# Optimization experiments

Hardware: AMD Instinct MI355X
Metric: run time of the kernel (lower is better)

## Reference

```python
import jax, jax.numpy as jnp
import numpy as np

N = 100000
E = 3200000
IN_DIM = 512
HID = 256
NUM_CLASSES = 16
P_DROP = 0.5
EPS_BN = 1e-5


def setup_inputs() -> dict:
    key = jax.random.key(0)
    ks = jax.random.split(key, 6)
    x = jax.random.normal(ks[0], (N, IN_DIM), jnp.float32)
    edge_src = jax.random.randint(ks[1], (E,), 0, N, dtype=jnp.int32)
    edge_dst = jax.random.randint(ks[2], (E,), 0, N, dtype=jnp.int32)
    # Glorot-ish init for GraphConv weights (bias=False in the module)
    W1 = jax.random.normal(ks[3], (IN_DIM, HID), jnp.float32) / np.sqrt(IN_DIM).astype(np.float32)
    W2 = jax.random.normal(ks[4], (HID, NUM_CLASSES), jnp.float32) / np.sqrt(HID).astype(np.float32)
    W3 = jax.random.normal(ks[5], (HID, NUM_CLASSES), jnp.float32) / np.sqrt(HID).astype(np.float32)
    return {"x": x, "W1": W1, "W2": W2, "W3": W3,
            "edge_src": edge_src, "edge_dst": edge_dst}


def _graph_conv(h, W, edge_src, edge_dst, out_inv_sqrt, in_inv_sqrt):
    # DGL GraphConv, norm='both', bias=False:
    #   rst = D_in^{-1/2} * A_agg( D_out^{-1/2} * h @ W )
    # Apply W before aggregation (out_dim <= in_dim here); same math as DGL.
    h = h * out_inv_sqrt[:, None]          # [N, d_in]
    h = h @ W                              # [N, d_out]
    agg = jax.ops.segment_sum(h[edge_src], edge_dst, num_segments=h.shape[0])
    return agg * in_inv_sqrt[:, None]


def _dropout(key, x, p=P_DROP):
    keep = jax.random.bernoulli(key, 1.0 - p, x.shape)
    return jnp.where(keep, x / (1.0 - p), jnp.zeros((), x.dtype))


def reference(x, W1, W2, W3, edge_src, edge_dst):
    n = x.shape[0]
    ones = jnp.ones(edge_src.shape[0], x.dtype)
    out_deg = jax.ops.segment_sum(ones, edge_src, num_segments=n)
    in_deg = jax.ops.segment_sum(ones, edge_dst, num_segments=n)
    out_is = jnp.maximum(out_deg, 1.0) ** -0.5   # DGL clamps degree to min 1
    in_is = jnp.maximum(in_deg, 1.0) ** -0.5

    k1, k2a, k2b, keps = jax.random.split(jax.random.key(42), 4)

    # gc1 + relu
    h = _dropout(k1, x)
    h = jax.nn.relu(_graph_conv(h, W1, edge_src, edge_dst, out_is, in_is))

    # BatchNorm1d(affine=False, track_running_stats=False): batch stats
    mean = jnp.mean(h, axis=0)
    var = jnp.var(h, axis=0)
    h = (h - mean) * jax.lax.rsqrt(var + EPS_BN)

    # gc2 (mu) and gc3 (logvar), each with its own dropout of hidden1
    mu = _graph_conv(_dropout(k2a, h), W2, edge_src, edge_dst, out_is, in_is)
    logvar = _graph_conv(_dropout(k2b, h), W3, edge_src, edge_dst, out_is, in_is)

    # reparameterize (training): eps * exp(logvar) + mu  (note: exp(logvar), per source)
    eps = jax.random.normal(keps, mu.shape, mu.dtype)
    return eps * jnp.exp(logvar) + mu
```

## Files before the change

kernel.cpp:

```cpp
#include <hip/hip_runtime.h>
#include <stdint.h>

#define N_NODES 100000
#define N_EDGES 3200000
#define IN_DIM  512
#define HID     256
#define NCLS    16

#define DBLK   256
#define DCHUNK (N_EDGES / DBLK)
#define DWIN2  50000

typedef unsigned short u16;
typedef __attribute__((ext_vector_type(8))) short short8;
typedef __attribute__((ext_vector_type(4))) float float4v;

__device__ __forceinline__ float bf2f(u16 u) {
  return __uint_as_float(((uint32_t)u) << 16);
}
__device__ __forceinline__ u16 f2bf(float f) {
  uint32_t u = __float_as_uint(f);
  return (u16)((u + 0x7fffu + ((u >> 16) & 1u)) >> 16);
}
__device__ __forceinline__ void acc8(float* a, uint4 v) {
  a[0] += bf2f((u16)(v.x & 0xffffu)); a[1] += bf2f((u16)(v.x >> 16));
  a[2] += bf2f((u16)(v.y & 0xffffu)); a[3] += bf2f((u16)(v.y >> 16));
  a[4] += bf2f((u16)(v.z & 0xffffu)); a[5] += bf2f((u16)(v.z >> 16));
  a[6] += bf2f((u16)(v.w & 0xffffu)); a[7] += bf2f((u16)(v.w >> 16));
}

__device__ __forceinline__ void gload16(const void* g, void* l) {
  __builtin_amdgcn_global_load_lds(
      (const __attribute__((address_space(1))) uint32_t*)g,
      (__attribute__((address_space(3))) uint32_t*)l, 16, 0, 0);
}

__host__ __device__ __forceinline__ uint32_t rotl32(uint32_t v, int d) {
  return (v << d) | (v >> (32 - d));
}

__host__ __device__ __forceinline__ void threefry2x32(uint32_t k0, uint32_t k1,
    uint32_t x0, uint32_t x1, uint32_t& o0, uint32_t& o1) {
  uint32_t ks0 = k0, ks1 = k1, ks2 = k0 ^ k1 ^ 0x1BD11BDAu;
  x0 += ks0; x1 += ks1;
#define TF_R(r) { x0 += x1; x1 = rotl32(x1, r); x1 ^= x0; }
  TF_R(13) TF_R(15) TF_R(26) TF_R(6)
  x0 += ks1; x1 += ks2 + 1u;
  TF_R(17) TF_R(29) TF_R(16) TF_R(24)
  x0 += ks2; x1 += ks0 + 2u;
  TF_R(13) TF_R(15) TF_R(26) TF_R(6)
  x0 += ks0; x1 += ks1 + 3u;
  TF_R(17) TF_R(29) TF_R(16) TF_R(24)
  x0 += ks1; x1 += ks2 + 4u;
  TF_R(13) TF_R(15) TF_R(26) TF_R(6)
  x0 += ks2; x1 += ks0 + 5u;
#undef TF_R
  o0 = x0; o1 = x1;
}

__host__ __device__ __forceinline__ uint32_t tf_bits32(uint32_t k0, uint32_t k1, uint32_t idx) {
  uint32_t o0, o1;
  threefry2x32(k0, k1, 0u, idx, o0, o1);
  return o0 ^ o1;
}

__device__ __forceinline__ float erfinv_f32(float x) {
  float w = -log1pf(-x * x);
  float p;
  if (w < 5.0f) {
    w -= 2.5f;
    p = 2.81022636e-08f;
    p = fmaf(p, w, 3.43273939e-07f);
    p = fmaf(p, w, -3.5233877e-06f);
    p = fmaf(p, w, -4.39150654e-06f);
    p = fmaf(p, w, 0.00021858087f);
    p = fmaf(p, w, -0.00125372503f);
    p = fmaf(p, w, -0.00417768164f);
    p = fmaf(p, w, 0.246640727f);
    p = fmaf(p, w, 1.50140941f);
  } else {
    w = sqrtf(w) - 3.0f;
    p = -0.000200214257f;
    p = fmaf(p, w, 0.000100950558f);
    p = fmaf(p, w, 0.00134934322f);
    p = fmaf(p, w, -0.00367342844f);
    p = fmaf(p, w, 0.00573950773f);
    p = fmaf(p, w, -0.0076224613f);
    p = fmaf(p, w, 0.00943887047f);
    p = fmaf(p, w, 1.00167406f);
    p = fmaf(p, w, 2.83297682f);
  }
  return p * x;
}

__global__ __launch_bounds__(1024) void hist_k(
    const int* __restrict__ esrc, const int* __restrict__ edst,
    u16* __restrict__ P16) {
  __shared__ uint32_t h32[DWIN2 / 2];
  const int b = blockIdx.x, tid = threadIdx.x;
  const int ebase = b * DCHUNK;
  for (int w = 0; w < 2; ++w) {
    const int lo = w * DWIN2;
    for (int i = tid; i < DWIN2 / 2; i += 1024) h32[i] = 0u;
    __syncthreads();
    for (int e = ebase + tid; e < ebase + DCHUNK; e += 1024) {
      int s = esrc[e], d = edst[e];
      unsigned su = (unsigned)(s - lo);
      if (su < (unsigned)DWIN2) atomicAdd(&h32[su >> 1], 1u << ((su & 1) * 16));
      unsigned du = (unsigned)(d - lo);
      if (du < (unsigned)DWIN2) atomicAdd(&h32[du >> 1], 0x100u << ((du & 1) * 16));
    }
    __syncthreads();
    for (int i = tid; i < DWIN2 / 2; i += 1024) {
      *(uint32_t*)(P16 + (size_t)b * N_NODES + lo + 2 * i) = h32[i];
    }
    __syncthreads();
  }
}

__global__ void degsum_k(u16* __restrict__ P16, int* __restrict__ ind,
                         float* __restrict__ out_is, float* __restrict__ in_is) {
  int n = blockIdx.x * 256 + threadIdx.x;
  if (n >= N_NODES) return;
  uint32_t to = 0, ti = 0;
#pragma unroll 8
  for (int b = 0; b < DBLK; ++b) {
    uint32_t v = P16[(size_t)b * N_NODES + n];
    P16[(size_t)b * N_NODES + n] = (u16)ti;
    to += v & 0xffu; ti += v >> 8;
  }
  ind[n] = (int)ti;
  out_is[n] = rsqrtf(fmaxf((float)to, 1.0f));
  in_is[n]  = rsqrtf(fmaxf((float)ti, 1.0f));
}

__global__ __launch_bounds__(1024) void scan_offsets_k(
    const int* __restrict__ ind, int* __restrict__ row_ofs) {
  __shared__ int wsum[16];
  const int tid = threadIdx.x;
  const int lane = tid & 63, wv = tid >> 6;
  int running = 0;
  for (int base = 0; base < N_NODES; base += 1024) {
    const int i = base + tid;
    int v = (i < N_NODES) ? ind[i] : 0;
    int sc = v;
#pragma unroll
    for (int d = 1; d < 64; d <<= 1) {
      int t = __shfl_up(sc, d, 64);
      if (lane >= d) sc += t;
    }
    if (lane == 63) wsum[wv] = sc;
    __syncthreads();
    if (wv == 0) {
      int t = (lane < 16) ? wsum[lane] : 0;
#pragma unroll
      for (int d = 1; d < 16; d <<= 1) {
        int u = __shfl_up(t, d, 64);
        if (lane >= d) t += u;
      }
      if (lane < 16) wsum[lane] = t;
    }
    __syncthreads();
    int wbase = (wv > 0) ? wsum[wv - 1] : 0;
    if (i < N_NODES) row_ofs[i] = running + wbase + sc - v;
    running += wsum[15];
    __syncthreads();
  }
  if (tid == 0) row_ofs[N_NODES] = running;
}

__global__ __launch_bounds__(1024) void place_k(
    const int* __restrict__ esrc, const int* __restrict__ edst,
    const u16* __restrict__ P16, const int* __restrict__ row_ofs,
    int* __restrict__ csr) {
  __shared__ uint32_t cur32[N_NODES / 4];
  const int b = blockIdx.x, tid = threadIdx.x;
  for (int i = tid; i < N_NODES / 4; i += 1024) cur32[i] = 0u;
  __syncthreads();
  const int ebase = b * DCHUNK;
  for (int e = ebase + tid; e < ebase + DCHUNK; e += 1024) {
    int d = edst[e];
    int base = row_ofs[d] + (int)P16[(size_t)b * N_NODES + d];
    uint32_t old = atomicAdd(&cur32[d >> 2], 1u << ((d & 3) * 8));
    int c = (int)((old >> ((d & 3) * 8)) & 0xffu);
    csr[base + c] = esrc[e];
  }
}

__global__ void gen_mask2_k(uint32_t ka0, uint32_t ka1, uint32_t kb0, uint32_t kb1,
                            uint32_t* __restrict__ maska, uint32_t* __restrict__ maskb) {
  uint32_t idx = blockIdx.x * blockDim.x + threadIdx.x;
  uint32_t ba = tf_bits32(ka0, ka1, idx);
  uint32_t bb = tf_bits32(kb0, kb1, idx);
  unsigned long long bala = __ballot((ba >> 31) == 0u);
  unsigned long long balb = __ballot((bb >> 31) == 0u);
  if ((threadIdx.x & 63) == 0) {
    uint32_t w = idx >> 5;
    maska[w] = (uint32_t)bala;
    maska[w + 1] = (uint32_t)(bala >> 32);
    maskb[w] = (uint32_t)balb;
    maskb[w + 1] = (uint32_t)(balb >> 32);
  }
}

__global__ __launch_bounds__(256) void cast_x_k(
    const float* __restrict__ x, const float* __restrict__ out_is,
    uint32_t k0, uint32_t k1, u16* __restrict__ Xb) {
  uint32_t t = blockIdx.x * 256u + threadIdx.x;
  uint32_t idx = t * 8u;
  uint32_t row = idx >> 9;
  float sc = 2.0f * out_is[row];
  float4 v0 = *(const float4*)(x + idx);
  float4 v1 = *(const float4*)(x + idx + 4);
  float vv[8] = {v0.x, v0.y, v0.z, v0.w, v1.x, v1.y, v1.z, v1.w};
  u16 o[8];
#pragma unroll
  for (int j = 0; j < 8; ++j) {
    uint32_t bits = tf_bits32(k0, k1, idx + (uint32_t)j);
    float val = (bits >> 31) ? 0.0f : vv[j] * sc;
    o[j] = f2bf(val);
  }
  uint4 pk;
  pk.x = (uint32_t)o[0] | ((uint32_t)o[1] << 16);
  pk.y = (uint32_t)o[2] | ((uint32_t)o[3] << 16);
  pk.z = (uint32_t)o[4] | ((uint32_t)o[5] << 16);
  pk.w = (uint32_t)o[6] | ((uint32_t)o[7] << 16);
  *(uint4*)(Xb + idx) = pk;
}

__global__ void cast_w_k(const float* __restrict__ W1, const float* __restrict__ W2,
                         const float* __restrict__ W3, u16* __restrict__ W1t,
                         u16* __restrict__ Wt23) {
  int idx = blockIdx.x * blockDim.x + threadIdx.x;
  if (idx < IN_DIM * HID) {
    int k = idx >> 8, n = idx & 255;
    W1t[n * IN_DIM + k] = f2bf(W1[idx]);
  } else {
    int t = idx - IN_DIM * HID;
    int n = t >> 8, k = t & 255;
    float v = (n < 16) ? W2[k * NCLS + n] : W3[k * NCLS + (n - 16)];
    Wt23[n * HID + k] = f2bf(v);
  }
}

#define G1_BM 128
#define G1_BKC 8
__global__ __launch_bounds__(512, 2) void gemm1_k(
    const u16* __restrict__ Xb, const u16* __restrict__ W1t, u16* __restrict__ X1b) {
  __shared__ u16 As[G1_BM * 64];
  __shared__ u16 Bs[256 * 64];
  const int tid = threadIdx.x;
  const int wid = tid >> 6, lane = tid & 63;
  const int wr = wid >> 2, wc = wid & 3;
  const int m16 = lane & 15, q = lane >> 4;
  const int srow = lane >> 3, schunk = lane & 7;
  const long base_row = (long)blockIdx.x * G1_BM;

  float4v acc[4][4];
#pragma unroll
  for (int i = 0; i < 4; ++i)
#pragma unroll
    for (int j = 0; j < 4; ++j) acc[i][j] = (float4v)0.0f;

  for (int ks = 0; ks < IN_DIM / 64; ++ks) {
#pragma unroll
    for (int i = 0; i < 2; ++i) {
      int j = wid * 2 + i;
      int row = j * 8 + srow;
      int gch = ks * G1_BKC + (schunk ^ (row & 7));
      gload16(Xb + (base_row + row) * IN_DIM + gch * 8, As + j * 512);
    }
#pragma unroll
    for (int i = 0; i < 4; ++i) {
      int j = wid * 4 + i;
      int n = j * 8 + srow;
      int gch = ks * G1_BKC + (schunk ^ (n & 7));
      gload16(W1t + (size_t)n * IN_DIM + gch * 8, Bs + j * 512);
    }
    __syncthreads();
#pragma unroll
    for (int kk = 0; kk < 2; ++kk) {
      short8 a[4], b[4];
      const int kq = kk * 4 + q;
      const int c = kq ^ (m16 & 7);
#pragma unroll
      for (int rt = 0; rt < 4; ++rt) {
        int row = wr * 64 + rt * 16 + m16;
        a[rt] = *(const short8*)(As + row * 64 + c * 8);
      }
#pragma unroll
      for (int ct = 0; ct < 4; ++ct) {
        int n = wc * 64 + ct * 16 + m16;
        b[ct] = *(const short8*)(Bs + n * 64 + c * 8);
      }
#pragma unroll
      for (int rt = 0; rt < 4; ++rt)
#pragma unroll
        for (int ct = 0; ct < 4; ++ct)
          acc[rt][ct] = __builtin_amdgcn_mfma_f32_16x16x32_bf16(a[rt], b[ct], acc[rt][ct], 0, 0, 0);
    }
    __syncthreads();
  }
#pragma unroll
  for (int rt = 0; rt < 4; ++rt) {
#pragma unroll
    for (int r = 0; r < 4; ++r) {
      long grow = base_row + wr * 64 + rt * 16 + q * 4 + r;
      if (grow < N_NODES) {
#pragma unroll
        for (int ct = 0; ct < 4; ++ct)
          X1b[grow * HID + wc * 64 + ct * 16 + m16] = f2bf(acc[rt][ct][r]);
      }
    }
  }
}

__global__ __launch_bounds__(256) void agg_relu_k(
    const u16* __restrict__ X1b, const int* __restrict__ row_ofs,
    const int* __restrict__ csr, const float* __restrict__ in_is,
    u16* __restrict__ h1b) {
  int d = blockIdx.x * 4 + (threadIdx.x >> 6);
  int lane = threadIdx.x & 63;
  int half = lane >> 5;
  int col = (lane & 31) * 8;
  int beg = row_ofs[d], end = row_ofs[d + 1];
  float a[8];
#pragma unroll
  for (int i = 0; i < 8; ++i) a[i] = 0.0f;
  int j = beg + half;
  for (; j + 14 < end; j += 16) {
    int s0 = csr[j],      s1 = csr[j + 2],  s2 = csr[j + 4],  s3 = csr[j + 6];
    int s4 = csr[j + 8],  s5 = csr[j + 10], s6 = csr[j + 12], s7 = csr[j + 14];
    uint4 v0 = *(const uint4*)(X1b + (size_t)s0 * HID + col);
    uint4 v1 = *(const uint4*)(X1b + (size_t)s1 * HID + col);
    uint4 v2 = *(const uint4*)(X1b + (size_t)s2 * HID + col);
    uint4 v3 = *(const uint4*)(X1b + (size_t)s3 * HID + col);
    uint4 v4 = *(const uint4*)(X1b + (size_t)s4 * HID + col);
    uint4 v5 = *(const uint4*)(X1b + (size_t)s5 * HID + col);
    uint4 v6 = *(const uint4*)(X1b + (size_t)s6 * HID + col);
    uint4 v7 = *(const uint4*)(X1b + (size_t)s7 * HID + col);
    acc8(a, v0); acc8(a, v1); acc8(a, v2); acc8(a, v3);
    acc8(a, v4); acc8(a, v5); acc8(a, v6); acc8(a, v7);
  }
  for (; j + 6 < end; j += 8) {
    int s0 = csr[j], s1 = csr[j + 2], s2 = csr[j + 4], s3 = csr[j + 6];
    uint4 v0 = *(const uint4*)(X1b + (size_t)s0 * HID + col);
    uint4 v1 = *(const uint4*)(X1b + (size_t)s1 * HID + col);
    uint4 v2 = *(const uint4*)(X1b + (size_t)s2 * HID + col);
    uint4 v3 = *(const uint4*)(X1b + (size_t)s3 * HID + col);
    acc8(a, v0); acc8(a, v1); acc8(a, v2); acc8(a, v3);
  }
  for (; j < end; j += 2) {
    uint4 v0 = *(const uint4*)(X1b + (size_t)csr[j] * HID + col);
    acc8(a, v0);
  }
#pragma unroll
  for (int i = 0; i < 8; ++i) a[i] += __shfl(a[i], lane ^ 32, 64);
  if (half == 0) {
    float is = in_is[d];
    u16 o[8];
#pragma unroll
    for (int i = 0; i < 8; ++i) o[i] = f2bf(fmaxf(a[i] * is, 0.0f));
    uint4 pk;
    pk.x = (uint32_t)o[0] | ((uint32_t)o[1] << 16);
    pk.y = (uint32_t)o[2] | ((uint32_t)o[3] << 16);
    pk.z = (uint32_t)o[4] | ((uint32_t)o[5] << 16);
    pk.w = (uint32_t)o[6] | ((uint32_t)o[7] << 16);
    *(uint4*)(h1b + (size_t)d * HID + col) = pk;
  }
}

__global__ __launch_bounds__(256) void bn_stats_k(const u16* __restrict__ h1b,
                                                  float* __restrict__ bn) {
  __shared__ float ls[512];
  const int tid = threadIdx.x;
  const int cb = (tid & 31) * 8;
  const int ms = tid >> 5;
  float s[8], s2[8];
#pragma unroll
  for (int i = 0; i < 8; ++i) { s[i] = 0.f; s2[i] = 0.f; }
  for (int m = ms;; m += 8) {
    int r = blockIdx.x + 256 * m;
    if (r >= N_NODES) break;
    uint4 v = *(const uint4*)(h1b + (size_t)r * HID + cb);
    float f[8];
    f[0] = bf2f((u16)(v.x & 0xffffu)); f[1] = bf2f((u16)(v.x >> 16));
    f[2] = bf2f((u16)(v.y & 0xffffu)); f[3] = bf2f((u16)(v.y >> 16));
    f[4] = bf2f((u16)(v.z & 0xffffu)); f[5] = bf2f((u16)(v.z >> 16));
    f[6] = bf2f((u16)(v.w & 0xffffu)); f[7] = bf2f((u16)(v.w >> 16));
#pragma unroll
    for (int i = 0; i < 8; ++i) { s[i] += f[i]; s2[i] += f[i] * f[i]; }
  }
  ls[tid] = 0.f; ls[tid + 256] = 0.f;
  __syncthreads();
#pragma unroll
  for (int i = 0; i < 8; ++i) {
    atomicAdd(&ls[cb + i], s[i]);
    atomicAdd(&ls[256 + cb + i], s2[i]);
  }
  __syncthreads();
  atomicAdd(&bn[tid], ls[tid]);
  atomicAdd(&bn[HID + tid], ls[256 + tid]);
}

__global__ void bn_fin_k(float* __restrict__ bn) {
  int c = threadIdx.x;
  float mean = bn[c] / (float)N_NODES;
  float var = bn[HID + c] / (float)N_NODES - mean * mean;
  float istd = rsqrtf(var + 1e-5f);
  bn[512 + c] = istd;
  bn[768 + c] = -mean * istd;
}

#define WLS 264
__global__ __launch_bounds__(256) void gemm23_k(
    const u16* __restrict__ h1b, const u16* __restrict__ Wt23,
    const uint32_t* __restrict__ mask2a, const uint32_t* __restrict__ mask2b,
    const float* __restrict__ out_is, const float* __restrict__ bn,
    u16* __restrict__ XMLV) {
  __shared__ u16 Wls[32 * WLS];
  __shared__ float cB[HID], cA[HID];
  const int tid = threadIdx.x;
#pragma unroll
  for (int i = 0; i < 4; ++i) {
    int idx = tid + i * 256;
    int n = idx >> 5, c = idx & 31;
    *(uint4*)(Wls + n * WLS + c * 8) = ((const uint4*)Wt23)[idx];
  }
  cB[tid] = bn[512 + tid];
  cA[tid] = bn[768 + tid];
  __syncthreads();

  const int wv = tid >> 6, lane = tid & 63;
  const int m = lane & 15, q = lane >> 4;
  const long arow = (long)blockIdx.x * 64 + wv * 16 + m;
  const bool valid = arow < N_NODES;
  const float osc = valid ? 2.0f * out_is[arow] : 0.0f;

  float4v accM = (float4v)0.0f, accL = (float4v)0.0f;
  for (int kc = 0; kc < HID; kc += 32) {
    const int kof = kc + q * 8;
    uint4 hv = make_uint4(0, 0, 0, 0);
    uint32_t wa = 0, wb = 0;
    if (valid) {
      hv = *(const uint4*)(h1b + arow * HID + kof);
      uint32_t widx = ((uint32_t)arow * HID + (uint32_t)kc) >> 5;
      wa = mask2a[widx] >> (q * 8);
      wb = mask2b[widx] >> (q * 8);
    }
    float4 B0 = *(const float4*)(cB + kof);
    float4 B1 = *(const float4*)(cB + kof + 4);
    float4 A0 = *(const float4*)(cA + kof);
    float4 A1 = *(const float4*)(cA + kof + 4);
    float hval[8] = {
      bf2f((u16)(hv.x & 0xffffu)), bf2f((u16)(hv.x >> 16)),
      bf2f((u16)(hv.y & 0xffffu)), bf2f((u16)(hv.y >> 16)),
      bf2f((u16)(hv.z & 0xffffu)), bf2f((u16)(hv.z >> 16)),
      bf2f((u16)(hv.w & 0xffffu)), bf2f((u16)(hv.w >> 16))};
    float nb[8] = {B0.x, B0.y, B0.z, B0.w, B1.x, B1.y, B1.z, B1.w};
    float na[8] = {A0.x, A0.y, A0.z, A0.w, A1.x, A1.y, A1.z, A1.w};
    short8 Aa, Ab;
#pragma unroll
    for (int jj = 0; jj < 8; ++jj) {
      float t = fmaf(hval[jj], nb[jj], na[jj]) * osc;
      u16 tb = f2bf(t);
      Aa[jj] = (short)(((wa >> jj) & 1u) ? tb : 0);
      Ab[jj] = (short)(((wb >> jj) & 1u) ? tb : 0);
    }
    short8 Bm = *(const short8*)(Wls + m * WLS + kof);
    short8 Bl = *(const short8*)(Wls + (16 + m) * WLS + kof);
    accM = __builtin_amdgcn_mfma_f32_16x16x32_bf16(Aa, Bm, accM, 0, 0, 0);
    accL = __builtin_amdgcn_mfma_f32_16x16x32_bf16(Ab, Bl, accL, 0, 0, 0);
  }
#pragma unroll
  for (int r = 0; r < 4; ++r) {
    long srow = (long)blockIdx.x * 64 + wv * 16 + q * 4 + r;
    if (srow < N_NODES) {
      XMLV[srow * 32 + m]      = f2bf(accM[r]);
      XMLV[srow * 32 + 16 + m] = f2bf(accL[r]);
    }
  }
}

__global__ __launch_bounds__(256) void agg_final_k(
    const u16* __restrict__ XMLV, const int* __restrict__ row_ofs,
    const int* __restrict__ csr, const float* __restrict__ in_is,
    uint32_t ke0, uint32_t ke1, float* __restrict__ out) {
  int g = blockIdx.x * 4 + (threadIdx.x >> 6);
  int lane = threadIdx.x & 63;
  int half = lane >> 5, c = lane & 31;
  int beg = row_ofs[g], end = row_ofs[g + 1];
  float s = 0.f;
  int j = beg + half;
  for (; j + 14 < end; j += 16) {
    int s0 = csr[j],      s1 = csr[j + 2],  s2 = csr[j + 4],  s3 = csr[j + 6];
    int s4 = csr[j + 8],  s5 = csr[j + 10], s6 = csr[j + 12], s7 = csr[j + 14];
    float v0 = bf2f(XMLV[(size_t)s0 * 32 + c]);
    float v1 = bf2f(XMLV[(size_t)s1 * 32 + c]);
    float v2 = bf2f(XMLV[(size_t)s2 * 32 + c]);
    float v3 = bf2f(XMLV[(size_t)s3 * 32 + c]);
    float v4 = bf2f(XMLV[(size_t)s4 * 32 + c]);
    float v5 = bf2f(XMLV[(size_t)s5 * 32 + c]);
    float v6 = bf2f(XMLV[(size_t)s6 * 32 + c]);
    float v7 = bf2f(XMLV[(size_t)s7 * 32 + c]);
    s += v0; s += v1; s += v2; s += v3;
    s += v4; s += v5; s += v6; s += v7;
  }
#pragma unroll
  for (int k = 0; k < 8; ++k) {
    int e = j + 2 * k;
    if (e < end) s += bf2f(XMLV[(size_t)csr[e] * 32 + c]);
  }
  s += __shfl(s, lane ^ 32, 64);
  if (half == 0) {
    s *= in_is[g];
    float other = __shfl(s, lane ^ 16, 64);
    if (c < 16) {
      uint32_t i = (uint32_t)(g * NCLS + c);
      uint32_t bits = tf_bits32(ke0, ke1, i);
      float f = __uint_as_float((bits >> 9) | 0x3f800000u) - 1.0f;
      const float lo = -0.99999994f;
      float u = fmaxf(lo, fmaf(f, 2.0f, lo));
      float eps = 1.41421356f * erfinv_f32(u);
      out[i] = eps * expf(other) + s;
    }
  }
}

extern "C" void kernel_launch(void* const* d_in, const int* in_sizes, int n_in,
                              void* d_out, int out_size, void* d_ws, size_t ws_size,
                              hipStream_t stream) {
  (void)in_sizes; (void)n_in; (void)out_size; (void)ws_size;
  const float* x  = (const float*)d_in[0];
  const float* W1 = (const float*)d_in[1];
  const float* W2 = (const float*)d_in[2];
  const float* W3 = (const float*)d_in[3];
  const int* esrc = (const int*)d_in[4];
  const int* edst = (const int*)d_in[5];
  float* out = (float*)d_out;

  uint32_t kb[8];
  for (int j = 0; j < 4; ++j)
    threefry2x32(0u, 42u, 0u, (uint32_t)j, kb[2 * j], kb[2 * j + 1]);

  char* p = (char*)d_ws;
  auto take = [&](size_t bytes) -> void* {
    void* r = (void*)p;
    p += (bytes + 255) & ~(size_t)255;
    return r;
  };
  u16* Xb        = (u16*)take(sizeof(u16) * (size_t)N_NODES * IN_DIM);
  u16* X1b       = (u16*)take(sizeof(u16) * (size_t)N_NODES * HID);
  u16* h1b       = (u16*)take(sizeof(u16) * (size_t)N_NODES * HID);
  u16* XMLV      = (u16*)take(sizeof(u16) * (size_t)N_NODES * 32);
  u16* W1t       = (u16*)take(sizeof(u16) * (size_t)IN_DIM * HID);
  u16* Wt23      = (u16*)take(sizeof(u16) * 32 * HID);
  uint32_t* mask2a = (uint32_t*)take((size_t)N_NODES * HID / 8);
  uint32_t* mask2b = (uint32_t*)take((size_t)N_NODES * HID / 8);
  int* in_deg    = (int*)take(sizeof(int) * N_NODES);
  float* out_is  = (float*)take(sizeof(float) * N_NODES);
  float* in_is   = (float*)take(sizeof(float) * N_NODES);
  int* row_ofs   = (int*)take(sizeof(int) * (N_NODES + 1));
  int* csr       = (int*)take(sizeof(int) * N_EDGES);
  float* bn      = (float*)take(sizeof(float) * 1024);

  u16* P16 = (u16*)Xb;

  hipMemsetAsync(bn, 0, sizeof(float) * 512, stream);

  hist_k<<<DBLK, 1024, 0, stream>>>(esrc, edst, P16);
  degsum_k<<<(N_NODES + 255) / 256, 256, 0, stream>>>(P16, in_deg, out_is, in_is);
  scan_offsets_k<<<1, 1024, 0, stream>>>(in_deg, row_ofs);
  place_k<<<DBLK, 1024, 0, stream>>>(esrc, edst, P16, row_ofs, csr);

  gen_mask2_k<<<(N_NODES * HID) / 256, 256, 0, stream>>>(kb[2], kb[3], kb[4], kb[5],
                                                         mask2a, mask2b);

  cast_w_k<<<(IN_DIM * HID + 32 * HID) / 256, 256, 0, stream>>>(W1, W2, W3, W1t, Wt23);
  cast_x_k<<<(N_NODES * IN_DIM / 8) / 256, 256, 0, stream>>>(x, out_is, kb[0], kb[1], Xb);

  gemm1_k<<<(N_NODES + G1_BM - 1) / G1_BM, 512, 0, stream>>>(Xb, W1t, X1b);
  agg_relu_k<<<N_NODES / 4, 256, 0, stream>>>(X1b, row_ofs, csr, in_is, h1b);
  bn_stats_k<<<256, 256, 0, stream>>>(h1b, bn);
  bn_fin_k<<<1, 256, 0, stream>>>(bn);
  gemm23_k<<<(N_NODES + 63) / 64, 256, 0, stream>>>(h1b, Wt23, mask2a, mask2b, out_is, bn, XMLV);
  agg_final_k<<<N_NODES / 4, 256, 0, stream>>>(XMLV, row_ofs, csr, in_is, kb[6], kb[7], out);
}
```

Before: 1.015 ms.

## Fuse dropout/cast into gemm1, inline dropout masks and BN finalize into gemm23

The x dropout plus bf16 cast is moved into gemm1's A-tile load, so the separate bf16 copy of x is no longer written and read back. The precomputed dropout bitmasks for the second layer are replaced by on-the-fly threefry generation inside gemm23. The BN finalize step is also folded into gemm23's prologue, which removes three kernel launches and several intermediate buffers. In exchange, gemm1 does synchronous fp32 loads and RNG work on the critical path with no async prefetch, and gemm23 now runs heavy RNG arithmetic per element.

Result: no change. 1.019 ms (+0.4%).

```diff
diff --git a/kernel.cpp b/kernel.cpp
--- a/kernel.cpp
+++ b/kernel.cpp
@@ -187,47 +187,6 @@
   }
 }
 
-__global__ void gen_mask2_k(uint32_t ka0, uint32_t ka1, uint32_t kb0, uint32_t kb1,
-                            uint32_t* __restrict__ maska, uint32_t* __restrict__ maskb) {
-  uint32_t idx = blockIdx.x * blockDim.x + threadIdx.x;
-  uint32_t ba = tf_bits32(ka0, ka1, idx);
-  uint32_t bb = tf_bits32(kb0, kb1, idx);
-  unsigned long long bala = __ballot((ba >> 31) == 0u);
-  unsigned long long balb = __ballot((bb >> 31) == 0u);
-  if ((threadIdx.x & 63) == 0) {
-    uint32_t w = idx >> 5;
-    maska[w] = (uint32_t)bala;
-    maska[w + 1] = (uint32_t)(bala >> 32);
-    maskb[w] = (uint32_t)balb;
-    maskb[w + 1] = (uint32_t)(balb >> 32);
-  }
-}
-
-__global__ __launch_bounds__(256) void cast_x_k(
-    const float* __restrict__ x, const float* __restrict__ out_is,
-    uint32_t k0, uint32_t k1, u16* __restrict__ Xb) {
-  uint32_t t = blockIdx.x * 256u + threadIdx.x;
-  uint32_t idx = t * 8u;
-  uint32_t row = idx >> 9;
-  float sc = 2.0f * out_is[row];
-  float4 v0 = *(const float4*)(x + idx);
-  float4 v1 = *(const float4*)(x + idx + 4);
-  float vv[8] = {v0.x, v0.y, v0.z, v0.w, v1.x, v1.y, v1.z, v1.w};
-  u16 o[8];
-#pragma unroll
-  for (int j = 0; j < 8; ++j) {
-    uint32_t bits = tf_bits32(k0, k1, idx + (uint32_t)j);
-    float val = (bits >> 31) ? 0.0f : vv[j] * sc;
-    o[j] = f2bf(val);
-  }
-  uint4 pk;
-  pk.x = (uint32_t)o[0] | ((uint32_t)o[1] << 16);
-  pk.y = (uint32_t)o[2] | ((uint32_t)o[3] << 16);
-  pk.z = (uint32_t)o[4] | ((uint32_t)o[5] << 16);
-  pk.w = (uint32_t)o[6] | ((uint32_t)o[7] << 16);
-  *(uint4*)(Xb + idx) = pk;
-}
-
 __global__ void cast_w_k(const float* __restrict__ W1, const float* __restrict__ W2,
                          const float* __restrict__ W3, u16* __restrict__ W1t,
                          u16* __restrict__ Wt23) {
@@ -246,7 +205,9 @@
 #define G1_BM 128
 #define G1_BKC 8
 __global__ __launch_bounds__(512, 2) void gemm1_k(
-    const u16* __restrict__ Xb, const u16* __restrict__ W1t, u16* __restrict__ X1b) {
+    const float* __restrict__ x, const float* __restrict__ out_is,
+    uint32_t k0, uint32_t k1,
+    const u16* __restrict__ W1t, u16* __restrict__ X1b) {
   __shared__ u16 As[G1_BM * 64];
   __shared__ u16 Bs[256 * 64];
   const int tid = threadIdx.x;
@@ -256,6 +217,14 @@
   const int srow = lane >> 3, schunk = lane & 7;
   const long base_row = (long)blockIdx.x * G1_BM;
 
+  const int arow_l = tid >> 2, acp = tid & 3;
+  const long agrow = base_row + arow_l;
+  const long asrow = (agrow < N_NODES) ? agrow : (N_NODES - 1);
+  const float asc = 2.0f * out_is[asrow];
+  const float* xrow = x + asrow * IN_DIM;
+  const int aw0 = ((2 * acp)     ^ (arow_l & 7)) * 8;
+  const int aw1 = ((2 * acp + 1) ^ (arow_l & 7)) * 8;
+
   float4v acc[4][4];
 #pragma unroll
   for (int i = 0; i < 4; ++i)
@@ -263,13 +232,31 @@
     for (int j = 0; j < 4; ++j) acc[i][j] = (float4v)0.0f;
 
   for (int ks = 0; ks < IN_DIM / 64; ++ks) {
-#pragma unroll
-    for (int i = 0; i < 2; ++i) {
-      int j = wid * 2 + i;
-      int row = j * 8 + srow;
-      int gch = ks * G1_BKC + (schunk ^ (row & 7));
-      gload16(Xb + (base_row + row) * IN_DIM + gch * 8, As + j * 512);
-    }
+    const int kbase = ks * 64 + acp * 16;
+    float4 f0 = *(const float4*)(xrow + kbase);
+    float4 f1 = *(const float4*)(xrow + kbase + 4);
+    float4 f2 = *(const float4*)(xrow + kbase + 8);
+    float4 f3 = *(const float4*)(xrow + kbase + 12);
+    float xv[16] = {f0.x, f0.y, f0.z, f0.w, f1.x, f1.y, f1.z, f1.w,
+                    f2.x, f2.y, f2.z, f2.w, f3.x, f3.y, f3.z, f3.w};
+    const uint32_t ibase = (uint32_t)asrow * IN_DIM + (uint32_t)kbase;
+    u16 ob[16];
+#pragma unroll
+    for (int j = 0; j < 16; ++j) {
+      uint32_t bits = tf_bits32(k0, k1, ibase + (uint32_t)j);
+      ob[j] = f2bf((bits >> 31) ? 0.0f : xv[j] * asc);
+    }
+    uint4 pka, pkb;
+    pka.x = (uint32_t)ob[0] | ((uint32_t)ob[1] << 16);
+    pka.y = (uint32_t)ob[2] | ((uint32_t)ob[3] << 16);
+    pka.z = (uint32_t)ob[4] | ((uint32_t)ob[5] << 16);
+    pka.w = (uint32_t)ob[6] | ((uint32_t)ob[7] << 16);
+    pkb.x = (uint32_t)ob[8] | ((uint32_t)ob[9] << 16);
+    pkb.y = (uint32_t)ob[10] | ((uint32_t)ob[11] << 16);
+    pkb.z = (uint32_t)ob[12] | ((uint32_t)ob[13] << 16);
+    pkb.w = (uint32_t)ob[14] | ((uint32_t)ob[15] << 16);
+    *(uint4*)(As + arow_l * 64 + aw0) = pka;
+    *(uint4*)(As + arow_l * 64 + aw1) = pkb;
 #pragma unroll
     for (int i = 0; i < 4; ++i) {
       int j = wid * 4 + i;
@@ -403,19 +390,10 @@
   atomicAdd(&bn[HID + tid], ls[256 + tid]);
 }
 
-__global__ void bn_fin_k(float* __restrict__ bn) {
-  int c = threadIdx.x;
-  float mean = bn[c] / (float)N_NODES;
-  float var = bn[HID + c] / (float)N_NODES - mean * mean;
-  float istd = rsqrtf(var + 1e-5f);
-  bn[512 + c] = istd;
-  bn[768 + c] = -mean * istd;
-}
-
 #define WLS 264
 __global__ __launch_bounds__(256) void gemm23_k(
     const u16* __restrict__ h1b, const u16* __restrict__ Wt23,
-    const uint32_t* __restrict__ mask2a, const uint32_t* __restrict__ mask2b,
+    uint32_t ka0, uint32_t ka1, uint32_t kb0, uint32_t kb1,
     const float* __restrict__ out_is, const float* __restrict__ bn,
     u16* __restrict__ XMLV) {
   __shared__ u16 Wls[32 * WLS];
@@ -427,8 +405,13 @@
     int n = idx >> 5, c = idx & 31;
     *(uint4*)(Wls + n * WLS + c * 8) = ((const uint4*)Wt23)[idx];
   }
-  cB[tid] = bn[512 + tid];
-  cA[tid] = bn[768 + tid];
+  {
+    float mean = bn[tid] * (1.0f / (float)N_NODES);
+    float var = bn[HID + tid] * (1.0f / (float)N_NODES) - mean * mean;
+    float istd = rsqrtf(var + 1e-5f);
+    cB[tid] = istd;
+    cA[tid] = -mean * istd;
+  }
   __syncthreads();
 
   const int wv = tid >> 6, lane = tid & 63;
@@ -436,18 +419,13 @@
   const long arow = (long)blockIdx.x * 64 + wv * 16 + m;
   const bool valid = arow < N_NODES;
   const float osc = valid ? 2.0f * out_is[arow] : 0.0f;
+  const uint32_t rbase = (uint32_t)(valid ? arow : 0) * HID;
 
   float4v accM = (float4v)0.0f, accL = (float4v)0.0f;
   for (int kc = 0; kc < HID; kc += 32) {
     const int kof = kc + q * 8;
     uint4 hv = make_uint4(0, 0, 0, 0);
-    uint32_t wa = 0, wb = 0;
-    if (valid) {
-      hv = *(const uint4*)(h1b + arow * HID + kof);
-      uint32_t widx = ((uint32_t)arow * HID + (uint32_t)kc) >> 5;
-      wa = mask2a[widx] >> (q * 8);
-      wb = mask2b[widx] >> (q * 8);
-    }
+    if (valid) hv = *(const uint4*)(h1b + arow * HID + kof);
     float4 B0 = *(const float4*)(cB + kof);
     float4 B1 = *(const float4*)(cB + kof + 4);
     float4 A0 = *(const float4*)(cA + kof);
@@ -459,13 +437,16 @@
       bf2f((u16)(hv.w & 0xffffu)), bf2f((u16)(hv.w >> 16))};
     float nb[8] = {B0.x, B0.y, B0.z, B0.w, B1.x, B1.y, B1.z, B1.w};
     float na[8] = {A0.x, A0.y, A0.z, A0.w, A1.x, A1.y, A1.z, A1.w};
+    const uint32_t ibase = rbase + (uint32_t)kof;
     short8 Aa, Ab;
 #pragma unroll
     for (int jj = 0; jj < 8; ++jj) {
       float t = fmaf(hval[jj], nb[jj], na[jj]) * osc;
       u16 tb = f2bf(t);
-      Aa[jj] = (short)(((wa >> jj) & 1u) ? tb : 0);
-      Ab[jj] = (short)(((wb >> jj) & 1u) ? tb : 0);
+      uint32_t ba = tf_bits32(ka0, ka1, ibase + (uint32_t)jj);
+      uint32_t bb = tf_bits32(kb0, kb1, ibase + (uint32_t)jj);
+      Aa[jj] = (short)((ba >> 31) ? 0 : tb);
+      Ab[jj] = (short)((bb >> 31) ? 0 : tb);
     }
     short8 Bm = *(const short8*)(Wls + m * WLS + kof);
     short8 Bl = *(const short8*)(Wls + (16 + m) * WLS + kof);
@@ -549,14 +530,12 @@
     p += (bytes + 255) & ~(size_t)255;
     return r;
   };
-  u16* Xb        = (u16*)take(sizeof(u16) * (size_t)N_NODES * IN_DIM);
+  u16* P16       = (u16*)take(sizeof(u16) * (size_t)DBLK * N_NODES);
   u16* X1b       = (u16*)take(sizeof(u16) * (size_t)N_NODES * HID);
   u16* h1b       = (u16*)take(sizeof(u16) * (size_t)N_NODES * HID);
   u16* XMLV      = (u16*)take(sizeof(u16) * (size_t)N_NODES * 32);
   u16* W1t       = (u16*)take(sizeof(u16) * (size_t)IN_DIM * HID);
   u16* Wt23      = (u16*)take(sizeof(u16) * 32 * HID);
-  uint32_t* mask2a = (uint32_t*)take((size_t)N_NODES * HID / 8);
-  uint32_t* mask2b = (uint32_t*)take((size_t)N_NODES * HID / 8);
   int* in_deg    = (int*)take(sizeof(int) * N_NODES);
   float* out_is  = (float*)take(sizeof(float) * N_NODES);
   float* in_is   = (float*)take(sizeof(float) * N_NODES);
@@ -564,8 +543,6 @@
   int* csr       = (int*)take(sizeof(int) * N_EDGES);
   float* bn      = (float*)take(sizeof(float) * 1024);
 
-  u16* P16 = (u16*)Xb;
-
   hipMemsetAsync(bn, 0, sizeof(float) * 512, stream);
 
   hist_k<<<DBLK, 1024, 0, stream>>>(esrc, edst, P16);
@@ -573,16 +550,12 @@
   scan_offsets_k<<<1, 1024, 0, stream>>>(in_deg, row_ofs);
   place_k<<<DBLK, 1024, 0, stream>>>(esrc, edst, P16, row_ofs, csr);
 
-  gen_mask2_k<<<(N_NODES * HID) / 256, 256, 0, stream>>>(kb[2], kb[3], kb[4], kb[5],
-                                                         mask2a, mask2b);
-
   cast_w_k<<<(IN_DIM * HID + 32 * HID) / 256, 256, 0, stream>>>(W1, W2, W3, W1t, Wt23);
-  cast_x_k<<<(N_NODES * IN_DIM / 8) / 256, 256, 0, stream>>>(x, out_is, kb[0], kb[1], Xb);
-
-  gemm1_k<<<(N_NODES + G1_BM - 1) / G1_BM, 512, 0, stream>>>(Xb, W1t, X1b);
+
+  gemm1_k<<<(N_NODES + G1_BM - 1) / G1_BM, 512, 0, stream>>>(x, out_is, kb[0], kb[1], W1t, X1b);
   agg_relu_k<<<N_NODES / 4, 256, 0, stream>>>(X1b, row_ofs, csr, in_is, h1b);
   bn_stats_k<<<256, 256, 0, stream>>>(h1b, bn);
-  bn_fin_k<<<1, 256, 0, stream>>>(bn);
-  gemm23_k<<<(N_NODES + 63) / 64, 256, 0, stream>>>(h1b, Wt23, mask2a, mask2b, out_is, bn, XMLV);
+  gemm23_k<<<(N_NODES + 63) / 64, 256, 0, stream>>>(h1b, Wt23, kb[2], kb[3], kb[4], kb[5],
+                                                    out_is, bn, XMLV);
   agg_final_k<<<N_NODES / 4, 256, 0, stream>>>(XMLV, row_ofs, csr, in_is, kb[6], kb[7], out);
 }
```
